# Kernel optimization log

Measured on AMD Instinct MI355X. Metric: run time of the kernel, lower is better.

Reference implementation:

```python
import jax, jax.numpy as jnp
import numpy as np

ORDER = 63
CODEBOOK_SIZE = 256
MIN_DATA = 1
N_ITER = 5
EPS = 1e-05
PERTURB = 1e-05


def setup_inputs() -> dict:
    key = jax.random.key(0)
    x = jax.random.normal(key, (131072, ORDER + 1), dtype=jnp.float32)
    return {"x": x}


def _e_step(x, cb, T):
    # squared euclidean distances via gram trick: (T, curr)
    d2 = jnp.sum(x * x, 1)[:, None] - 2.0 * (x @ cb.T) + jnp.sum(cb * cb, 1)[None, :]
    idx = jnp.argmin(d2, axis=1)
    xq = cb[idx]
    dist = jnp.sum((x - xq) ** 2) / T
    return idx, dist


def _m_step(x, idx, curr, key):
    D = x.shape[1]
    ones = jnp.ones((x.shape[0],), x.dtype)
    n_data = jax.ops.segment_sum(ones, idx, num_segments=curr)        # histc
    mask = n_data >= MIN_DATA
    sums = jax.ops.segment_sum(x, idx, num_segments=curr)             # scatter_add
    cent = sums / jnp.maximum(n_data, 1.0)[:, None]
    m = jnp.argmax(n_data)
    r = jax.random.normal(key, (curr, D), x.dtype) * PERTURB
    nm = (~mask).astype(x.dtype)
    # empty clusters reseeded from the largest cluster, perturbed
    new = jnp.where(mask[:, None], cent, cent[m][None, :] - r)
    cnt = jnp.sum(nm)
    corr = jnp.sum(r * nm[:, None], axis=0) / jnp.maximum(cnt, 1.0)
    new = new.at[m].add(jnp.where(cnt > 0, corr, jnp.zeros_like(corr)))
    return new


def _lbg(x):
    T, D = x.shape
    K = CODEBOOK_SIZE
    codebook = jnp.full((K, D), 1e10, x.dtype).at[0].set(jnp.mean(x, axis=0))
    distance = jnp.asarray(jnp.inf, x.dtype)
    base = jax.random.key(42)
    curr = 1
    split = 0
    while curr * 2 <= K:  # static loop over log2(K) binary splits
        key_s = jax.random.fold_in(base, split)
        kr, kloop = jax.random.split(key_s)
        r = jax.random.normal(kr, (curr, D), x.dtype) * PERTURB
        codebook = codebook.at[curr:2 * curr].set(codebook[:curr] - r).at[:curr].add(r)
        curr *= 2
        prev = distance

        def body(carry, n, curr=curr):
            cb, prev_d, dist, done, key = carry
            idx, d_new = _e_step(x, cb, T)
            change = jnp.abs(prev_d - d_new)
            conv = (n > 0) & (change / (d_new + 1e-16) < EPS)
            key, sub = jax.random.split(key)
            cb_new = _m_step(x, idx, curr, sub)
            stop = done | conv
            cb_out = jnp.where(stop, cb, cb_new)        # skip m-step on convergence/break
            dist_out = jnp.where(done, dist, d_new)     # distance assigned before break
            prev_out = jnp.where(stop, prev_d, d_new)
            return (cb_out, prev_out, dist_out, stop, key), None

        carry0 = (codebook[:curr], prev, distance, jnp.asarray(False), kloop)
        (cb_fin, _, distance, _, _), _ = jax.lax.scan(body, carry0, jnp.arange(N_ITER))
        codebook = codebook.at[:curr].set(cb_fin)
        split += 1
    return codebook, distance


def reference(x):
    return _lbg(x)
```

## Files before the change

kernel.cpp:

```cpp
#include <hip/hip_runtime.h>
#include <stdint.h>


#define NPTS 131072
#define DIMS 64
#define KCB  256

struct LbgState { float dist; float prev; unsigned int done; unsigned int k0, k1; unsigned int pad; };

__device__ __forceinline__ uint32_t rotl32(uint32_t v, int n){ return (v<<n)|(v>>(32-n)); }

__device__ __forceinline__ void tf2x32(uint32_t k0, uint32_t k1, uint32_t x0, uint32_t x1,
                                       uint32_t& o0, uint32_t& o1){
  uint32_t ks2 = k0 ^ k1 ^ 0x1BD11BDAu;
  x0 += k0; x1 += k1;
  #define TFR(r) { x0 += x1; x1 = rotl32(x1, r); x1 ^= x0; }
  TFR(13) TFR(15) TFR(26) TFR(6)
  x0 += k1; x1 += ks2 + 1u;
  TFR(17) TFR(29) TFR(16) TFR(24)
  x0 += ks2; x1 += k0 + 2u;
  TFR(13) TFR(15) TFR(26) TFR(6)
  x0 += k0; x1 += k1 + 3u;
  TFR(17) TFR(29) TFR(16) TFR(24)
  x0 += k1; x1 += ks2 + 4u;
  TFR(13) TFR(15) TFR(26) TFR(6)
  x0 += ks2; x1 += k0 + 5u;
  #undef TFR
  o0 = x0; o1 = x1;
}

__device__ __forceinline__ float xla_erfinv_f32(float x){
  float w = -log1pf(-x*x);
  float p;
  if (w < 5.0f){
    w = w - 2.5f;
    p = 2.81022636e-08f;
    p = fmaf(p, w, 3.43273939e-07f);
    p = fmaf(p, w, -3.5233877e-06f);
    p = fmaf(p, w, -4.39150654e-06f);
    p = fmaf(p, w, 0.00021858087f);
    p = fmaf(p, w, -0.00125372503f);
    p = fmaf(p, w, -0.00417768164f);
    p = fmaf(p, w, 0.246640727f);
    p = fmaf(p, w, 1.50140941f);
  } else {
    w = sqrtf(w) - 3.0f;
    p = -0.000200214257f;
    p = fmaf(p, w, 0.000100950558f);
    p = fmaf(p, w, 0.00134934322f);
    p = fmaf(p, w, -0.00367342844f);
    p = fmaf(p, w, 0.00573950773f);
    p = fmaf(p, w, -0.0076224613f);
    p = fmaf(p, w, 0.00943887047f);
    p = fmaf(p, w, 1.00167406f);
    p = fmaf(p, w, 2.83297682f);
  }
  return p * x;
}

__device__ __forceinline__ float jax_normal_elem(uint32_t k0, uint32_t k1, uint32_t j){
  uint32_t o0, o1; tf2x32(k0, k1, 0u, j, o0, o1);
  uint32_t bits = o0 ^ o1;
  uint32_t fb = (bits >> 9) | 0x3f800000u;
  float f = __uint_as_float(fb) - 1.0f;
  const float lo = -0.99999994f;
  float u = f * 2.0f + lo;
  u = fmaxf(lo, u);
  return 1.41421356f * xla_erfinv_f32(u);
}

__device__ void do_split(float* __restrict__ cb, float* __restrict__ cnorm,
                         unsigned long long* __restrict__ sums,
                         unsigned int* __restrict__ ndata,
                         unsigned long long* __restrict__ distacc,
                         LbgState* __restrict__ st, int curr, int split, int t){
  __shared__ uint32_t kr0s, kr1s;
  if (t == 0){
    uint32_t ks0, ks1, a0, a1, b0, b1;
    tf2x32(0u, 42u, 0u, (uint32_t)split, ks0, ks1);
    tf2x32(ks0, ks1, 0u, 0u, a0, a1);
    tf2x32(ks0, ks1, 0u, 1u, b0, b1);
    kr0s = a0; kr1s = a1;
    st->k0 = b0; st->k1 = b1;
    st->prev = st->dist;
    st->done = 0u;
  }
  __syncthreads();
  const int n = curr * DIMS;
  for (int e = t; e < n; e += 256){
    int c = e >> 6, d = e & 63;
    float rv = jax_normal_elem(kr0s, kr1s, (uint32_t)e) * 1e-5f;
    float old = cb[c*DIMS + d];
    cb[(curr + c)*DIMS + d] = old - rv;
    cb[c*DIMS + d]          = old + rv;
  }
  __syncthreads();
  const int c2 = curr * 2;
  for (int c = t; c < c2; c += 256){
    float s = 0.f;
    for (int d = 0; d < DIMS; d++){ float vv = cb[c*DIMS+d]; s += vv*vv; }
    cnorm[c] = s;
  }
  for (int e = t; e < c2*DIMS; e += 256) sums[e] = 0ull;
  for (int c = t; c < c2; c += 256) ndata[c] = 0u;
  if (t == 0) *distacc = 0ull;
}

__global__ void mean_kernel(const float* __restrict__ x, unsigned long long* __restrict__ macc,
                            float* __restrict__ cb, float* __restrict__ cnorm,
                            unsigned long long* __restrict__ sums,
                            unsigned int* __restrict__ ndata,
                            unsigned long long* __restrict__ distacc,
                            LbgState* __restrict__ st, unsigned int* __restrict__ mcnt){
  __shared__ double part[256];
  __shared__ float stage[16*64];
  __shared__ int islast;
  const int t = threadIdx.x;
  const int d = t & 63;
  const int w = t >> 6;
  const size_t base = (size_t)blockIdx.x * 1024;
  const int lrow = t >> 4;
  const int lcol = (t & 15) * 4;

  const float4* xg = reinterpret_cast<const float4*>(x);
  float4 nxt = xg[((base + lrow) * DIMS + lcol) >> 2];
  double s = 0.0;
  for (int tt = 0; tt < 64; tt++){
    float4 cur = nxt;
    if (tt < 63)
      nxt = xg[((base + (tt+1)*16 + lrow) * DIMS + lcol) >> 2];
    __syncthreads();
    *reinterpret_cast<float4*>(&stage[lrow*DIMS + lcol]) = cur;
    __syncthreads();
    s += (double)stage[(w    )*DIMS + d];
    s += (double)stage[(w + 4)*DIMS + d];
    s += (double)stage[(w + 8)*DIMS + d];
    s += (double)stage[(w +12)*DIMS + d];
  }
  part[t] = s;
  __syncthreads();
  if (t < 64){
    double tot = part[t] + part[64+t] + part[128+t] + part[192+t];
    atomicAdd(&macc[t], (unsigned long long)__double2ll_rn(tot * 1099511627776.0));
  }
  __threadfence();
  __syncthreads();
  if (t == 0) islast = (atomicAdd(mcnt, 1u) == (unsigned)(gridDim.x - 1));
  __syncthreads();
  if (!islast) return;

  if (t < 64){
    long long mv = (long long)atomicAdd(&macc[t], 0ull);
    double mean = (double)mv * (1.0/1099511627776.0) / 131072.0;
    cb[t] = (float)mean;
  }
  for (int e = t; e < KCB*DIMS; e += 256)
    if (e >= 64) cb[e] = 1e10f;
  if (t == 0){
    st->dist = __builtin_inff();
    st->prev = __builtin_inff();
    st->done = 0u;
    atomicExch(mcnt, 0u);
  }
  __syncthreads();
  do_split(cb, cnorm, sums, ndata, distacc, st, 1, 0, t);
}

template<int CURR>
__global__ __launch_bounds__(256, 4)
void estep_kernel(const float* __restrict__ x, const float* __restrict__ cb,
                  const float* __restrict__ cnorm, unsigned char* __restrict__ bidx8,
                  unsigned long long* __restrict__ distacc, const LbgState* __restrict__ st){
  if (st->done) return;
  const int t = threadIdx.x;
  const int lane = t & 63;
  const int p = blockIdx.x * 256 + t;

  float xv[DIMS];
  const float4* xp = reinterpret_cast<const float4*>(x + (size_t)p * DIMS);
  #pragma unroll
  for (int i = 0; i < 16; i++){
    float4 v = xp[i];
    xv[4*i+0] = v.x; xv[4*i+1] = v.y; xv[4*i+2] = v.z; xv[4*i+3] = v.w;
  }
  float xx = 0.f;
  #pragma unroll
  for (int d = 0; d < DIMS; d++) xx += xv[d] * xv[d];

  constexpr int NJ = (CURR < 4) ? CURR : 4;
  float best = __builtin_inff();
  int bi = 0;
  for (int j0 = 0; j0 < CURR; j0 += NJ){
    const float* crow = cb + (size_t)j0 * DIMS;
    float acc[NJ];
    #pragma unroll
    for (int k = 0; k < NJ; k++) acc[k] = 0.f;
    #pragma unroll
    for (int d = 0; d < DIMS; d++){
      #pragma unroll
      for (int k = 0; k < NJ; k++)
        acc[k] = fmaf(xv[d], crow[k*DIMS + d], acc[k]);
    }
    #pragma unroll
    for (int k = 0; k < NJ; k++){
      float d2 = (xx - 2.0f*acc[k]) + cnorm[j0 + k];
      if (d2 < best){ best = d2; bi = j0 + k; }
    }
  }
  bidx8[p] = (unsigned char)bi;

  double dd = 0.0;
  const float4* cbv = reinterpret_cast<const float4*>(cb + (size_t)bi * DIMS);
  #pragma unroll
  for (int i = 0; i < 16; i++){
    float4 b = cbv[i];
    float df, sq;
    df = xv[4*i+0] - b.x; sq = df*df; dd += (double)sq;
    df = xv[4*i+1] - b.y; sq = df*df; dd += (double)sq;
    df = xv[4*i+2] - b.z; sq = df*df; dd += (double)sq;
    df = xv[4*i+3] - b.w; sq = df*df; dd += (double)sq;
  }
  for (int off = 32; off > 0; off >>= 1) dd += __shfl_down(dd, off);
  if (lane == 0)
    atomicAdd(distacc, (unsigned long long)__double2ll_rn(dd * 4294967296.0));
}

template<int CURR>
__global__ __launch_bounds__(256, 4)
void estep_sw(const float* __restrict__ x, const float* __restrict__ cb,
              const float* __restrict__ cnorm, unsigned char* __restrict__ bidx8,
              unsigned long long* __restrict__ distacc, const LbgState* __restrict__ st){
  if (st->done) return;
  constexpr int CPW = CURR / 4;
  constexpr int NJG = (CPW < 8) ? CPW : 8;
  constexpr int NG = CPW / NJG;
  __shared__ float4 xs[16*128];
  __shared__ float sxx[128];
  __shared__ float sbest[4*128];
  __shared__ int   sidx [4*128];
  __shared__ unsigned char sbidx[128];
  const int t = threadIdx.x;
  const int lane = t & 63;
  const int w = __builtin_amdgcn_readfirstlane(t >> 6);
  const int pbase = blockIdx.x * 128;

  {
    const int p = t & 127, h = t >> 7;
    const float4* xg = reinterpret_cast<const float4*>(x) + (size_t)(pbase + p) * 16 + h * 8;
    #pragma unroll
    for (int j = 0; j < 8; j++)
      xs[(h*8 + j)*128 + p] = xg[j];
  }
  __syncthreads();
  if (t < 128){
    float xx = 0.f;
    #pragma unroll
    for (int k4 = 0; k4 < 16; k4++){
      float4 v = xs[k4*128 + t];
      xx = fmaf(v.x, v.x, xx); xx = fmaf(v.y, v.y, xx);
      xx = fmaf(v.z, v.z, xx); xx = fmaf(v.w, v.w, xx);
    }
    sxx[t] = xx;
  }
  __syncthreads();

  const float xx0 = sxx[lane];
  const float xx1 = sxx[64 + lane];
  float best0 = __builtin_inff(), best1 = __builtin_inff();
  int bi0 = 0, bi1 = 0;
  const float4* cbg = reinterpret_cast<const float4*>(cb);
  const int cwbase = w * CPW;

  for (int g = 0; g < NG; g++){
    const int c0 = cwbase + g*NJG;
    float acc0[NJG], acc1[NJG];
    #pragma unroll
    for (int cj = 0; cj < NJG; cj++){ acc0[cj] = 0.f; acc1[cj] = 0.f; }
    for (int k4 = 0; k4 < 16; k4++){
      float4 xf0 = xs[k4*128 + lane];
      float4 xf1 = xs[k4*128 + 64 + lane];
      #pragma unroll
      for (int cj = 0; cj < NJG; cj++){
        float4 cf = cbg[(size_t)(c0 + cj)*16 + k4];
        acc0[cj] = fmaf(xf0.x, cf.x, acc0[cj]);
        acc0[cj] = fmaf(xf0.y, cf.y, acc0[cj]);
        acc0[cj] = fmaf(xf0.z, cf.z, acc0[cj]);
        acc0[cj] = fmaf(xf0.w, cf.w, acc0[cj]);
        acc1[cj] = fmaf(xf1.x, cf.x, acc1[cj]);
        acc1[cj] = fmaf(xf1.y, cf.y, acc1[cj]);
        acc1[cj] = fmaf(xf1.z, cf.z, acc1[cj]);
        acc1[cj] = fmaf(xf1.w, cf.w, acc1[cj]);
      }
    }
    #pragma unroll
    for (int cj = 0; cj < NJG; cj++){
      float cn = cnorm[c0 + cj];
      float d20 = (xx0 - 2.0f*acc0[cj]) + cn;
      if (d20 < best0){ best0 = d20; bi0 = c0 + cj; }
      float d21 = (xx1 - 2.0f*acc1[cj]) + cn;
      if (d21 < best1){ best1 = d21; bi1 = c0 + cj; }
    }
  }
  sbest[w*128 + lane]      = best0;  sidx[w*128 + lane]      = bi0;
  sbest[w*128 + 64 + lane] = best1;  sidx[w*128 + 64 + lane] = bi1;
  __syncthreads();

  if (t < 128){
    float best = sbest[t];
    int bi = sidx[t];
    #pragma unroll
    for (int ww = 1; ww < 4; ww++){
      float ob = sbest[ww*128 + t];
      int   oi = sidx [ww*128 + t];
      if (ob < best){ best = ob; bi = oi; }
    }
    sbidx[t] = (unsigned char)bi;
    bidx8[pbase + t] = (unsigned char)bi;
    const float4* cbv = cbg + (size_t)bi * 16;
    double dd = 0.0;
    #pragma unroll
    for (int k4 = 0; k4 < 16; k4++){
      float4 xv = xs[k4*128 + t];
      float4 b = cbv[k4];
      float df, sq;
      df = xv.x - b.x; sq = df*df; dd += (double)sq;
      df = xv.y - b.y; sq = df*df; dd += (double)sq;
      df = xv.z - b.z; sq = df*df; dd += (double)sq;
      df = xv.w - b.w; sq = df*df; dd += (double)sq;
    }
    for (int off = 32; off > 0; off >>= 1) dd += __shfl_down(dd, off);
    if ((t & 63) == 0)
      atomicAdd(distacc, (unsigned long long)__double2ll_rn(dd * 4294967296.0));
  }
}

template<int CURR, int NBLK>
__global__ __launch_bounds__(256)
void gather_kernel(const float* __restrict__ x, const unsigned char* __restrict__ bidx8,
                   unsigned long long* __restrict__ sums, unsigned int* __restrict__ ndata,
                   const LbgState* __restrict__ st){
  if (st->done) return;
  constexpr int CLOG = __builtin_ctz(CURR);
  constexpr int NCHUNK = NBLK / CURR;
  constexpr int PPC = NPTS / NCHUNK;
  constexpr int NPW = PPC / 4;
  __shared__ long long sacc[4*64];
  __shared__ unsigned int scw[4];
  const int t = threadIdx.x;
  const int lane = t & 63;
  const int w = t >> 6;
  const int c = blockIdx.x & (CURR - 1);
  const int chunk = blockIdx.x >> CLOG;
  const int pbase = chunk * PPC + w * NPW;

  long long acc = 0;
  unsigned int cnt = 0;
  int q0 = 0, q1 = 0, q2 = 0, q3 = 0, qn = 0;
  const uint32_t* bp = reinterpret_cast<const uint32_t*>(bidx8 + pbase);
  for (int i = 0; i < NPW; i += 256){
    const uint32_t b4 = bp[(i >> 2) + lane];
    #pragma unroll
    for (int s = 0; s < 4; s++){
      unsigned long long m = __ballot(((b4 >> (8*s)) & 255u) == (unsigned)c);
      cnt += (unsigned int)__popcll(m);
      while (m){
        const int bit = __builtin_ctzll(m);
        m &= m - 1ull;
        const int p = pbase + i + bit*4 + s;
        if      (qn == 0) q0 = p;
        else if (qn == 1) q1 = p;
        else if (qn == 2) q2 = p;
        else              q3 = p;
        qn++;
        if (qn == 4){
          const float v0 = x[(size_t)q0 * DIMS + lane];
          const float v1 = x[(size_t)q1 * DIMS + lane];
          const float v2 = x[(size_t)q2 * DIMS + lane];
          const float v3 = x[(size_t)q3 * DIMS + lane];
          acc += (long long)__double2int_rn((double)v0 * 1048576.0);
          acc += (long long)__double2int_rn((double)v1 * 1048576.0);
          acc += (long long)__double2int_rn((double)v2 * 1048576.0);
          acc += (long long)__double2int_rn((double)v3 * 1048576.0);
          qn = 0;
        }
      }
    }
  }
  if (qn > 0){
    const int i1 = (qn > 1) ? q1 : q0;
    const int i2 = (qn > 2) ? q2 : q0;
    const float v0 = x[(size_t)q0 * DIMS + lane];
    const float v1 = x[(size_t)i1 * DIMS + lane];
    const float v2 = x[(size_t)i2 * DIMS + lane];
    acc += (long long)__double2int_rn((double)v0 * 1048576.0);
    if (qn > 1) acc += (long long)__double2int_rn((double)v1 * 1048576.0);
    if (qn > 2) acc += (long long)__double2int_rn((double)v2 * 1048576.0);
  }
  sacc[w*64 + lane] = acc;
  if (lane == 0) scw[w] = cnt;
  __syncthreads();
  if (w == 0){
    long long tot = sacc[lane] + sacc[64+lane] + sacc[128+lane] + sacc[192+lane];
    if (tot) atomicAdd(&sums[c*DIMS + lane], (unsigned long long)(tot * 1048576ll));
    if (lane == 0){
      unsigned int ct = scw[0] + scw[1] + scw[2] + scw[3];
      if (ct) atomicAdd(&ndata[c], ct);
    }
  }
}

__global__ void control_kernel(float* __restrict__ cb, float* __restrict__ cnorm,
                               unsigned long long* __restrict__ sums,
                               unsigned int* __restrict__ ndata,
                               unsigned long long* __restrict__ distacc,
                               LbgState* __restrict__ st, int curr, int n_iter,
                               int next_split){
  __shared__ int s_stop;
  __shared__ unsigned int sdone;
  __shared__ uint32_t sub0, sub1;
  __shared__ float cm[64];
  __shared__ int redv[256];
  __shared__ int redi[256];
  __shared__ int s_m, s_cnt;
  const int t = threadIdx.x;
  if (t == 0) sdone = st->done;
  __syncthreads();
  const unsigned int done0 = sdone;

  if (!done0){
    if (t == 0){
      double dd = (double)(long long)(*distacc) * (1.0/4294967296.0);
      float sf = (float)dd;
      float d_new = sf / 131072.0f;
      float change = fabsf(st->prev - d_new);
      int conv = (n_iter > 0) && (change / (d_new + 1e-16f) < 1e-5f);
      st->dist = d_new;
      if (!conv) st->prev = d_new;
      st->done = conv ? 1u : 0u;
      s_stop = conv;
      if (!conv){
        uint32_t a0, a1, b0, b1;
        tf2x32(st->k0, st->k1, 0u, 0u, a0, a1);
        tf2x32(st->k0, st->k1, 0u, 1u, b0, b1);
        st->k0 = a0; st->k1 = a1;
        sub0 = b0; sub1 = b1;
      }
    }
    __syncthreads();
    if (!s_stop){
      int v = (t < curr) ? (int)ndata[t] : -1;
      redv[t] = v; redi[t] = t;
      __syncthreads();
      for (int s = 128; s > 0; s >>= 1){
        if (t < s){
          if (redv[t+s] > redv[t] || (redv[t+s] == redv[t] && redi[t+s] < redi[t])){
            redv[t] = redv[t+s]; redi[t] = redi[t+s];
          }
        }
        __syncthreads();
      }
      if (t == 0) s_m = redi[0];
      __syncthreads();
      redv[t] = (t < curr && ndata[t] == 0u) ? 1 : 0;
      __syncthreads();
      for (int s = 128; s > 0; s >>= 1){
        if (t < s) redv[t] += redv[t+s];
        __syncthreads();
      }
      if (t == 0) s_cnt = redv[0];
      __syncthreads();
      const int m = s_m;
      const int cntE = s_cnt;

      if (t < 64){
        unsigned int nm_ = ndata[m]; if (nm_ < 1u) nm_ = 1u;
        double cd = (double)(long long)sums[m*DIMS + t] * (1.0/1099511627776.0) / (double)nm_;
        cm[t] = (float)cd;
      }
      __syncthreads();

      const int total = curr * DIMS;
      for (int e = t; e < total; e += 256){
        int c = e >> 6, d = e & 63;
        if (c == m) continue;
        float nv;
        unsigned int nd = ndata[c];
        if (nd >= 1u){
          double cd = (double)(long long)sums[e] * (1.0/1099511627776.0) / (double)nd;
          nv = (float)cd;
        } else {
          float rv = jax_normal_elem(sub0, sub1, (uint32_t)e) * 1e-5f;
          nv = cm[d] - rv;
        }
        cb[e] = nv;
      }
      if (t < 64){
        float add = 0.f;
        if (cntE > 0){
          float acc = 0.f;
          for (int c = 0; c < curr; c++){
            if (ndata[c] == 0u)
              acc += jax_normal_elem(sub0, sub1, (uint32_t)(c*DIMS + t)) * 1e-5f;
          }
          add = acc / fmaxf((float)cntE, 1.0f);
        }
        cb[m*DIMS + t] = cm[t] + add;
      }
      __syncthreads();

      for (int c = t; c < curr; c += 256){
        float s = 0.f;
        for (int d = 0; d < DIMS; d++){ float vv = cb[c*DIMS+d]; s += vv*vv; }
        cnorm[c] = s;
      }
      for (int e = t; e < total; e += 256) sums[e] = 0ull;
      for (int c = t; c < curr; c += 256) ndata[c] = 0u;
      if (t == 0) *distacc = 0ull;
    }
  }
  __syncthreads();
  if (n_iter == 4){
    if (curr < 256){
      do_split(cb, cnorm, sums, ndata, distacc, st, curr, next_split, t);
    } else if (t == 0){
      cb[KCB*DIMS] = st->dist;
    }
  }
}

extern "C" void kernel_launch(void* const* d_in, const int* in_sizes, int n_in,
                              void* d_out, int out_size, void* d_ws, size_t ws_size,
                              hipStream_t stream){
  const float* x = (const float*)d_in[0];
  float* cb = (float*)d_out;
  char* ws = (char*)d_ws;
  unsigned long long* sums    = (unsigned long long*)(ws + 0);
  unsigned long long* macc    = (unsigned long long*)(ws + 131072);
  unsigned long long* distacc = (unsigned long long*)(ws + 131584);
  LbgState* st                = (LbgState*)(ws + 131592);
  unsigned int* ndata         = (unsigned int*)(ws + 131616);
  float* cnorm                = (float*)(ws + 132640);
  unsigned char* bidx8        = (unsigned char*)(ws + 133664);
  unsigned int* mcnt          = (unsigned int*)(ws + 264736);

  hipMemsetAsync(d_ws, 0, 264744, stream);
  mean_kernel<<<128, 256, 0, stream>>>(x, macc, cb, cnorm, sums, ndata, distacc, st, mcnt);

  for (int split = 0; split < 8; split++){
    const int curr = 2 << split;
    for (int n = 0; n < 5; n++){
      switch (curr){
        case 2:   estep_kernel<2>  <<<512,256,0,stream>>>(x,cb,cnorm,bidx8,distacc,st);
                  gather_kernel<2,256>   <<<256, 256,0,stream>>>(x,bidx8,sums,ndata,st); break;
        case 4:   estep_kernel<4>  <<<512,256,0,stream>>>(x,cb,cnorm,bidx8,distacc,st);
                  gather_kernel<4,512>   <<<512, 256,0,stream>>>(x,bidx8,sums,ndata,st); break;
        case 8:   estep_sw<8>    <<<1024,256,0,stream>>>(x,cb,cnorm,bidx8,distacc,st);
                  gather_kernel<8,1024>  <<<1024,256,0,stream>>>(x,bidx8,sums,ndata,st); break;
        case 16:  estep_sw<16>   <<<1024,256,0,stream>>>(x,cb,cnorm,bidx8,distacc,st);
                  gather_kernel<16,2048> <<<2048,256,0,stream>>>(x,bidx8,sums,ndata,st); break;
        case 32:  estep_sw<32>   <<<1024,256,0,stream>>>(x,cb,cnorm,bidx8,distacc,st);
                  gather_kernel<32,2048> <<<2048,256,0,stream>>>(x,bidx8,sums,ndata,st); break;
        case 64:  estep_sw<64>   <<<1024,256,0,stream>>>(x,cb,cnorm,bidx8,distacc,st);
                  gather_kernel<64,512>  <<<512, 256,0,stream>>>(x,bidx8,sums,ndata,st); break;
        case 128: estep_sw<128>  <<<1024,256,0,stream>>>(x,cb,cnorm,bidx8,distacc,st);
                  gather_kernel<128,1024><<<1024,256,0,stream>>>(x,bidx8,sums,ndata,st); break;
        case 256: estep_sw<256>  <<<1024,256,0,stream>>>(x,cb,cnorm,bidx8,distacc,st);
                  gather_kernel<256,2048><<<2048,256,0,stream>>>(x,bidx8,sums,ndata,st); break;
      }
      control_kernel<<<1, 256, 0, stream>>>(cb, cnorm, sums, ndata, distacc, st, curr, n, split+1);
    }
  }
}
```

Before: 3.112 ms.

## Fuse control kernel into gather kernel via last-block-done atomic counter

Removes the single-block control_kernel launch after each LBG iteration and folds its logic into the tail of the gather kernel, where the last block to finish (found with an acq_rel atomic counter) runs the M-step update, split and bookkeeping. The counts are cached in shared memory and sums read with agent-scope atomic loads. It also replaces the threadfence plus atomic pattern in the mean kernel with scoped acquire/release atomics. This saves 40 kernel launches and their gaps, at the cost of serialized tail work in one block and reliance on correct memory ordering.

```diff
diff --git a/kernel.cpp b/kernel.cpp
--- a/kernel.cpp
+++ b/kernel.cpp
@@ -143,14 +143,14 @@
     double tot = part[t] + part[64+t] + part[128+t] + part[192+t];
     atomicAdd(&macc[t], (unsigned long long)__double2ll_rn(tot * 1099511627776.0));
   }
-  __threadfence();
-  __syncthreads();
-  if (t == 0) islast = (atomicAdd(mcnt, 1u) == (unsigned)(gridDim.x - 1));
+  __syncthreads();
+  if (t == 0) islast = (__hip_atomic_fetch_add(mcnt, 1u, __ATOMIC_ACQ_REL,
+                                               __HIP_MEMORY_SCOPE_AGENT) == (unsigned)(gridDim.x - 1));
   __syncthreads();
   if (!islast) return;
 
   if (t < 64){
-    long long mv = (long long)atomicAdd(&macc[t], 0ull);
+    long long mv = (long long)__hip_atomic_load(&macc[t], __ATOMIC_RELAXED, __HIP_MEMORY_SCOPE_AGENT);
     double mean = (double)mv * (1.0/1099511627776.0) / 131072.0;
     cb[t] = (float)mean;
   }
@@ -160,7 +160,7 @@
     st->dist = __builtin_inff();
     st->prev = __builtin_inff();
     st->done = 0u;
-    atomicExch(mcnt, 0u);
+    __hip_atomic_store(mcnt, 0u, __ATOMIC_RELAXED, __HIP_MEMORY_SCOPE_AGENT);
   }
   __syncthreads();
   do_split(cb, cnorm, sums, ndata, distacc, st, 1, 0, t);
@@ -336,98 +336,99 @@
 
 template<int CURR, int NBLK>
 __global__ __launch_bounds__(256)
-void gather_kernel(const float* __restrict__ x, const unsigned char* __restrict__ bidx8,
-                   unsigned long long* __restrict__ sums, unsigned int* __restrict__ ndata,
-                   const LbgState* __restrict__ st){
-  if (st->done) return;
+void gatherc_kernel(const float* __restrict__ x, const unsigned char* __restrict__ bidx8,
+                    unsigned long long* __restrict__ sums, unsigned int* __restrict__ ndata,
+                    float* __restrict__ cb, float* __restrict__ cnorm,
+                    unsigned long long* __restrict__ distacc, LbgState* __restrict__ st,
+                    unsigned int* __restrict__ gcnt, int n_iter, int next_split){
   constexpr int CLOG = __builtin_ctz(CURR);
   constexpr int NCHUNK = NBLK / CURR;
   constexpr int PPC = NPTS / NCHUNK;
   constexpr int NPW = PPC / 4;
   __shared__ long long sacc[4*64];
   __shared__ unsigned int scw[4];
+  __shared__ int islast;
   const int t = threadIdx.x;
   const int lane = t & 63;
   const int w = t >> 6;
-  const int c = blockIdx.x & (CURR - 1);
-  const int chunk = blockIdx.x >> CLOG;
-  const int pbase = chunk * PPC + w * NPW;
-
-  long long acc = 0;
-  unsigned int cnt = 0;
-  int q0 = 0, q1 = 0, q2 = 0, q3 = 0, qn = 0;
-  const uint32_t* bp = reinterpret_cast<const uint32_t*>(bidx8 + pbase);
-  for (int i = 0; i < NPW; i += 256){
-    const uint32_t b4 = bp[(i >> 2) + lane];
-    #pragma unroll
-    for (int s = 0; s < 4; s++){
-      unsigned long long m = __ballot(((b4 >> (8*s)) & 255u) == (unsigned)c);
-      cnt += (unsigned int)__popcll(m);
-      while (m){
-        const int bit = __builtin_ctzll(m);
-        m &= m - 1ull;
-        const int p = pbase + i + bit*4 + s;
-        if      (qn == 0) q0 = p;
-        else if (qn == 1) q1 = p;
-        else if (qn == 2) q2 = p;
-        else              q3 = p;
-        qn++;
-        if (qn == 4){
-          const float v0 = x[(size_t)q0 * DIMS + lane];
-          const float v1 = x[(size_t)q1 * DIMS + lane];
-          const float v2 = x[(size_t)q2 * DIMS + lane];
-          const float v3 = x[(size_t)q3 * DIMS + lane];
-          acc += (long long)__double2int_rn((double)v0 * 1048576.0);
-          acc += (long long)__double2int_rn((double)v1 * 1048576.0);
-          acc += (long long)__double2int_rn((double)v2 * 1048576.0);
-          acc += (long long)__double2int_rn((double)v3 * 1048576.0);
-          qn = 0;
+  const unsigned int done0 = st->done;
+
+  if (!done0){
+    const int c = blockIdx.x & (CURR - 1);
+    const int chunk = blockIdx.x >> CLOG;
+    const int pbase = chunk * PPC + w * NPW;
+    long long acc = 0;
+    unsigned int cnt = 0;
+    int q0 = 0, q1 = 0, q2 = 0, q3 = 0, qn = 0;
+    const uint32_t* bp = reinterpret_cast<const uint32_t*>(bidx8 + pbase);
+    for (int i = 0; i < NPW; i += 256){
+      const uint32_t b4 = bp[(i >> 2) + lane];
+      #pragma unroll
+      for (int s = 0; s < 4; s++){
+        unsigned long long m = __ballot(((b4 >> (8*s)) & 255u) == (unsigned)c);
+        cnt += (unsigned int)__popcll(m);
+        while (m){
+          const int bit = __builtin_ctzll(m);
+          m &= m - 1ull;
+          const int p = pbase + i + bit*4 + s;
+          if      (qn == 0) q0 = p;
+          else if (qn == 1) q1 = p;
+          else if (qn == 2) q2 = p;
+          else              q3 = p;
+          qn++;
+          if (qn == 4){
+            const float v0 = x[(size_t)q0 * DIMS + lane];
+            const float v1 = x[(size_t)q1 * DIMS + lane];
+            const float v2 = x[(size_t)q2 * DIMS + lane];
+            const float v3 = x[(size_t)q3 * DIMS + lane];
+            acc += (long long)__double2int_rn((double)v0 * 1048576.0);
+            acc += (long long)__double2int_rn((double)v1 * 1048576.0);
+            acc += (long long)__double2int_rn((double)v2 * 1048576.0);
+            acc += (long long)__double2int_rn((double)v3 * 1048576.0);
+            qn = 0;
+          }
         }
       }
     }
-  }
-  if (qn > 0){
-    const int i1 = (qn > 1) ? q1 : q0;
-    const int i2 = (qn > 2) ? q2 : q0;
-    const float v0 = x[(size_t)q0 * DIMS + lane];
-    const float v1 = x[(size_t)i1 * DIMS + lane];
-    const float v2 = x[(size_t)i2 * DIMS + lane];
-    acc += (long long)__double2int_rn((double)v0 * 1048576.0);
-    if (qn > 1) acc += (long long)__double2int_rn((double)v1 * 1048576.0);
-    if (qn > 2) acc += (long long)__double2int_rn((double)v2 * 1048576.0);
-  }
-  sacc[w*64 + lane] = acc;
-  if (lane == 0) scw[w] = cnt;
-  __syncthreads();
-  if (w == 0){
-    long long tot = sacc[lane] + sacc[64+lane] + sacc[128+lane] + sacc[192+lane];
-    if (tot) atomicAdd(&sums[c*DIMS + lane], (unsigned long long)(tot * 1048576ll));
-    if (lane == 0){
-      unsigned int ct = scw[0] + scw[1] + scw[2] + scw[3];
-      if (ct) atomicAdd(&ndata[c], ct);
-    }
-  }
-}
-
-__global__ void control_kernel(float* __restrict__ cb, float* __restrict__ cnorm,
-                               unsigned long long* __restrict__ sums,
-                               unsigned int* __restrict__ ndata,
-                               unsigned long long* __restrict__ distacc,
-                               LbgState* __restrict__ st, int curr, int n_iter,
-                               int next_split){
+    if (qn > 0){
+      const int i1 = (qn > 1) ? q1 : q0;
+      const int i2 = (qn > 2) ? q2 : q0;
+      const float v0 = x[(size_t)q0 * DIMS + lane];
+      const float v1 = x[(size_t)i1 * DIMS + lane];
+      const float v2 = x[(size_t)i2 * DIMS + lane];
+      acc += (long long)__double2int_rn((double)v0 * 1048576.0);
+      if (qn > 1) acc += (long long)__double2int_rn((double)v1 * 1048576.0);
+      if (qn > 2) acc += (long long)__double2int_rn((double)v2 * 1048576.0);
+    }
+    sacc[w*64 + lane] = acc;
+    if (lane == 0) scw[w] = cnt;
+    __syncthreads();
+    if (w == 0){
+      long long tot = sacc[lane] + sacc[64+lane] + sacc[128+lane] + sacc[192+lane];
+      if (tot) atomicAdd(&sums[c*DIMS + lane], (unsigned long long)(tot * 1048576ll));
+      if (lane == 0){
+        unsigned int ct = scw[0] + scw[1] + scw[2] + scw[3];
+        if (ct) atomicAdd(&ndata[c], ct);
+      }
+    }
+  }
+  __syncthreads();
+  if (t == 0) islast = (__hip_atomic_fetch_add(gcnt, 1u, __ATOMIC_ACQ_REL,
+                                               __HIP_MEMORY_SCOPE_AGENT) == (unsigned)(NBLK - 1));
+  __syncthreads();
+  if (!islast) return;
+  if (t == 0) __hip_atomic_store(gcnt, 0u, __ATOMIC_RELAXED, __HIP_MEMORY_SCOPE_AGENT);
+
   __shared__ int s_stop;
-  __shared__ unsigned int sdone;
   __shared__ uint32_t sub0, sub1;
   __shared__ float cm[64];
   __shared__ int redv[256];
   __shared__ int redi[256];
   __shared__ int s_m, s_cnt;
-  const int t = threadIdx.x;
-  if (t == 0) sdone = st->done;
-  __syncthreads();
-  const unsigned int done0 = sdone;
-
+  __shared__ unsigned int snd[256];
   if (!done0){
+    if (t < CURR)
+      snd[t] = __hip_atomic_load(&ndata[t], __ATOMIC_RELAXED, __HIP_MEMORY_SCOPE_AGENT);
     if (t == 0){
       double dd = (double)(long long)(*distacc) * (1.0/4294967296.0);
       float sf = (float)dd;
@@ -448,7 +449,7 @@
     }
     __syncthreads();
     if (!s_stop){
-      int v = (t < curr) ? (int)ndata[t] : -1;
+      int v = (t < CURR) ? (int)snd[t] : -1;
       redv[t] = v; redi[t] = t;
       __syncthreads();
       for (int s = 128; s > 0; s >>= 1){
@@ -461,7 +462,7 @@
       }
       if (t == 0) s_m = redi[0];
       __syncthreads();
-      redv[t] = (t < curr && ndata[t] == 0u) ? 1 : 0;
+      redv[t] = (t < CURR && snd[t] == 0u) ? 1 : 0;
       __syncthreads();
       for (int s = 128; s > 0; s >>= 1){
         if (t < s) redv[t] += redv[t+s];
@@ -473,20 +474,24 @@
       const int cntE = s_cnt;
 
       if (t < 64){
-        unsigned int nm_ = ndata[m]; if (nm_ < 1u) nm_ = 1u;
-        double cd = (double)(long long)sums[m*DIMS + t] * (1.0/1099511627776.0) / (double)nm_;
+        unsigned int nm_ = snd[m]; if (nm_ < 1u) nm_ = 1u;
+        long long sv = (long long)__hip_atomic_load(&sums[m*DIMS + t], __ATOMIC_RELAXED,
+                                                    __HIP_MEMORY_SCOPE_AGENT);
+        double cd = (double)sv * (1.0/1099511627776.0) / (double)nm_;
         cm[t] = (float)cd;
       }
       __syncthreads();
 
-      const int total = curr * DIMS;
+      const int total = CURR * DIMS;
       for (int e = t; e < total; e += 256){
         int c = e >> 6, d = e & 63;
         if (c == m) continue;
         float nv;
-        unsigned int nd = ndata[c];
+        unsigned int nd = snd[c];
         if (nd >= 1u){
-          double cd = (double)(long long)sums[e] * (1.0/1099511627776.0) / (double)nd;
+          long long sv = (long long)__hip_atomic_load(&sums[e], __ATOMIC_RELAXED,
+                                                      __HIP_MEMORY_SCOPE_AGENT);
+          double cd = (double)sv * (1.0/1099511627776.0) / (double)nd;
           nv = (float)cd;
         } else {
           float rv = jax_normal_elem(sub0, sub1, (uint32_t)e) * 1e-5f;
@@ -498,8 +503,8 @@
         float add = 0.f;
         if (cntE > 0){
           float acc = 0.f;
-          for (int c = 0; c < curr; c++){
-            if (ndata[c] == 0u)
+          for (int c = 0; c < CURR; c++){
+            if (snd[c] == 0u)
               acc += jax_normal_elem(sub0, sub1, (uint32_t)(c*DIMS + t)) * 1e-5f;
           }
           add = acc / fmaxf((float)cntE, 1.0f);
@@ -508,20 +513,20 @@
       }
       __syncthreads();
 
-      for (int c = t; c < curr; c += 256){
+      for (int c = t; c < CURR; c += 256){
         float s = 0.f;
         for (int d = 0; d < DIMS; d++){ float vv = cb[c*DIMS+d]; s += vv*vv; }
         cnorm[c] = s;
       }
       for (int e = t; e < total; e += 256) sums[e] = 0ull;
-      for (int c = t; c < curr; c += 256) ndata[c] = 0u;
+      for (int c = t; c < CURR; c += 256) ndata[c] = 0u;
       if (t == 0) *distacc = 0ull;
     }
   }
   __syncthreads();
   if (n_iter == 4){
-    if (curr < 256){
-      do_split(cb, cnorm, sums, ndata, distacc, st, curr, next_split, t);
+    if (CURR < 256){
+      do_split(cb, cnorm, sums, ndata, distacc, st, CURR, next_split, t);
     } else if (t == 0){
       cb[KCB*DIMS] = st->dist;
     }
@@ -542,6 +547,7 @@
   float* cnorm                = (float*)(ws + 132640);
   unsigned char* bidx8        = (unsigned char*)(ws + 133664);
   unsigned int* mcnt          = (unsigned int*)(ws + 264736);
+  unsigned int* gcnt          = (unsigned int*)(ws + 264740);
 
   hipMemsetAsync(d_ws, 0, 264744, stream);
   mean_kernel<<<128, 256, 0, stream>>>(x, macc, cb, cnorm, sums, ndata, distacc, st, mcnt);
@@ -551,23 +557,22 @@
     for (int n = 0; n < 5; n++){
       switch (curr){
         case 2:   estep_kernel<2>  <<<512,256,0,stream>>>(x,cb,cnorm,bidx8,distacc,st);
-                  gather_kernel<2,256>   <<<256, 256,0,stream>>>(x,bidx8,sums,ndata,st); break;
+                  gatherc_kernel<2,256>   <<<256, 256,0,stream>>>(x,bidx8,sums,ndata,cb,cnorm,distacc,st,gcnt,n,split+1); break;
         case 4:   estep_kernel<4>  <<<512,256,0,stream>>>(x,cb,cnorm,bidx8,distacc,st);
-                  gather_kernel<4,512>   <<<512, 256,0,stream>>>(x,bidx8,sums,ndata,st); break;
+                  gatherc_kernel<4,512>   <<<512, 256,0,stream>>>(x,bidx8,sums,ndata,cb,cnorm,distacc,st,gcnt,n,split+1); break;
         case 8:   estep_sw<8>    <<<1024,256,0,stream>>>(x,cb,cnorm,bidx8,distacc,st);
-                  gather_kernel<8,1024>  <<<1024,256,0,stream>>>(x,bidx8,sums,ndata,st); break;
+                  gatherc_kernel<8,1024>  <<<1024,256,0,stream>>>(x,bidx8,sums,ndata,cb,cnorm,distacc,st,gcnt,n,split+1); break;
         case 16:  estep_sw<16>   <<<1024,256,0,stream>>>(x,cb,cnorm,bidx8,distacc,st);
-                  gather_kernel<16,2048> <<<2048,256,0,stream>>>(x,bidx8,sums,ndata,st); break;
+                  gatherc_kernel<16,2048> <<<2048,256,0,stream>>>(x,bidx8,sums,ndata,cb,cnorm,distacc,st,gcnt,n,split+1); break;
         case 32:  estep_sw<32>   <<<1024,256,0,stream>>>(x,cb,cnorm,bidx8,distacc,st);
-                  gather_kernel<32,2048> <<<2048,256,0,stream>>>(x,bidx8,sums,ndata,st); break;
+                  gatherc_kernel<32,2048> <<<2048,256,0,stream>>>(x,bidx8,sums,ndata,cb,cnorm,distacc,st,gcnt,n,split+1); break;
         case 64:  estep_sw<64>   <<<1024,256,0,stream>>>(x,cb,cnorm,bidx8,distacc,st);
-                  gather_kernel<64,512>  <<<512, 256,0,stream>>>(x,bidx8,sums,ndata,st); break;
+                  gatherc_kernel<64,512>  <<<512, 256,0,stream>>>(x,bidx8,sums,ndata,cb,cnorm,distacc,st,gcnt,n,split+1); break;
         case 128: estep_sw<128>  <<<1024,256,0,stream>>>(x,cb,cnorm,bidx8,distacc,st);
-                  gather_kernel<128,1024><<<1024,256,0,stream>>>(x,bidx8,sums,ndata,st); break;
+                  gatherc_kernel<128,1024><<<1024,256,0,stream>>>(x,bidx8,sums,ndata,cb,cnorm,distacc,st,gcnt,n,split+1); break;
         case 256: estep_sw<256>  <<<1024,256,0,stream>>>(x,cb,cnorm,bidx8,distacc,st);
-                  gather_kernel<256,2048><<<2048,256,0,stream>>>(x,bidx8,sums,ndata,st); break;
-      }
-      control_kernel<<<1, 256, 0, stream>>>(cb, cnorm, sums, ndata, distacc, st, curr, n, split+1);
-    }
-  }
-}
+                  gatherc_kernel<256,2048><<<2048,256,0,stream>>>(x,bidx8,sums,ndata,cb,cnorm,distacc,st,gcnt,n,split+1); break;
+      }
+    }
+  }
+}
```

After: 3.714 ms. 19.3% more time.
